# Performance work log

Measured on AMD Instinct MI355X. Metric: run time of the kernel, lower is better.

Reference implementation:

```python
import jax, jax.numpy as jnp
import numpy as np

B, S = 64, 1024
DC, DR, H, DA = 64, 64, 128, 128
NC, NQ, MC = 256, 10000, 4


def setup_inputs() -> dict:
    key = jax.random.key(0)
    ks = jax.random.split(key, 16)
    question_seq = jax.random.randint(ks[0], (B, S), 0, NQ)
    correctness_seq = jax.random.randint(ks[1], (B, S), 0, 2)
    q2c_table = jax.random.randint(ks[2], (NQ, MC), 0, NC)
    q2c_mask = jax.random.randint(ks[3], (NQ, MC), 0, 2).at[:, 0].set(1)  # >=1 concept per question
    sd = 0.02
    concept_embed = jax.random.normal(ks[4], (NC, DC), jnp.float32) * sd
    correctness_embed = jax.random.normal(ks[5], (2, DR), jnp.float32) * sd
    mlp_w = jax.random.normal(ks[6], (DA, H), jnp.float32) * (1.0 / np.sqrt(H))
    mlp_b = jnp.zeros((DA,), jnp.float32)
    sim_w = jax.random.normal(ks[7], (1, DA), jnp.float32) * (1.0 / np.sqrt(DA))
    DIN = DC + DR
    W_ih = jax.random.normal(ks[8], (3 * H, DIN), jnp.float32) * (1.0 / np.sqrt(H))
    b_ih = jnp.zeros((3 * H,), jnp.float32)
    W_hh = jax.random.normal(ks[9], (3 * H, H), jnp.float32) * (1.0 / np.sqrt(H))
    b_hh = jnp.zeros((3 * H,), jnp.float32)
    pred_w = jax.random.normal(ks[10], (1, 2 * H + DC), jnp.float32) * (1.0 / np.sqrt(2 * H + DC))
    pred_b = jnp.zeros((1,), jnp.float32)
    return dict(question_seq=question_seq, correctness_seq=correctness_seq,
                q2c_table=q2c_table, q2c_mask=q2c_mask,
                concept_embed=concept_embed, correctness_embed=correctness_embed,
                mlp_w=mlp_w, mlp_b=mlp_b, sim_w=sim_w,
                W_ih=W_ih, b_ih=b_ih, W_hh=W_hh, b_hh=b_hh,
                pred_w=pred_w, pred_b=pred_b)


def _concept_emb(question_seq, q2c_table, q2c_mask, concept_embed):
    # fused question->concept embedding: masked mean over mapped concepts
    cids = q2c_table[question_seq]                      # [B,S,MC]
    m = q2c_mask[question_seq].astype(jnp.float32)      # [B,S,MC]
    ce = concept_embed[cids]                            # [B,S,MC,DC]
    return (ce * m[..., None]).sum(2) / jnp.clip(m.sum(2), 1.0)[..., None]


def _gru(x, W_ih, b_ih, W_hh, b_hh):
    # torch nn.GRU equations, batch_first; x: [B,S,DIN] -> [B,S,H]
    Xp = jnp.einsum('bsd,gd->bsg', x, W_ih) + b_ih      # [B,S,3H]
    h0 = jnp.zeros((x.shape[0], H), x.dtype)

    def step(h, gi):
        gh = h @ W_hh.T + b_hh
        i_r, i_z, i_n = jnp.split(gi, 3, axis=-1)
        h_r, h_z, h_n = jnp.split(gh, 3, axis=-1)
        r = jax.nn.sigmoid(i_r + h_r)
        z = jax.nn.sigmoid(i_z + h_z)
        n = jnp.tanh(i_n + r * h_n)
        h_new = (1.0 - z) * n + z * h
        return h_new, h_new

    _, hs = jax.lax.scan(step, h0, Xp.transpose(1, 0, 2))
    return hs.transpose(1, 0, 2)


def _attention(rnn_out, mlp_w, mlp_b, sim_w):
    # additive per-key score, causal softmax, bmm, exclusive cumsum, concat
    s = jnp.einsum('bsa,oa->bso', jnp.tanh(jnp.einsum('bsh,ah->bsa', rnn_out, mlp_w) + mlp_b), sim_w)[..., 0]  # [B,S]
    seq = rnn_out.shape[1]
    causal = jnp.tril(jnp.ones((seq, seq), bool))       # keep j<=i
    scores = jnp.where(causal[None], s[:, None, :], -jnp.inf)  # [B,S,S]
    alphas = jax.nn.softmax(scores, axis=-1)
    attn = jnp.einsum('bij,bjh->bih', alphas, rnn_out)  # [B,S,H]
    excl = jnp.cumsum(attn, axis=1) - attn              # exclusive cumsum
    return jnp.concatenate([excl, rnn_out], axis=-1)    # [B,S,2H]


def reference(question_seq, correctness_seq, q2c_table, q2c_mask,
              concept_embed, correctness_embed, mlp_w, mlp_b, sim_w,
              W_ih, b_ih, W_hh, b_hh, pred_w, pred_b):
    concept = _concept_emb(question_seq, q2c_table, q2c_mask, concept_embed)  # [B,S,DC]
    corr = correctness_embed[correctness_seq]                                  # [B,S,DR]
    cc = jnp.concatenate([concept, corr], -1)
    rc = jnp.concatenate([corr, concept], -1)
    inter = jnp.where((correctness_seq == 1)[..., None], cc, rc)               # [B,S,DC+DR]
    rnn_out = _gru(inter, W_ih, b_ih, W_hh, b_hh)                              # [B,S,H]
    latent = _attention(rnn_out, mlp_w, mlp_b, sim_w)                          # [B,S,2H]
    pin = jnp.concatenate([latent[:, :-1], concept[:, 1:]], axis=-1)           # [B,S-1,2H+DC]
    logits = jnp.einsum('bsd,od->bso', pin, pred_w) + pred_b
    return jax.nn.sigmoid(logits)[..., 0]                                      # [B,S-1]
```

## Files before the change

### kernel.cpp

```cpp
#include <hip/hip_runtime.h>
#include <hip/hip_bf16.h>
#include <cstdint>

#define BB 64
#define SS 1024
#define DCn 64
#define Hn 128
#define G3 384
#define HPITCH 144

using f32x4 = __attribute__((ext_vector_type(4))) float;
using bf16x8 = __attribute__((ext_vector_type(8))) short;

__device__ __forceinline__ float sigmoid_f(float x) {
  return __builtin_amdgcn_rcpf(1.0f + __expf(-x));
}
__device__ __forceinline__ float tanh_f(float x) {
  float xc = fminf(fmaxf(x, -15.0f), 15.0f);
  float t = __expf(-2.0f * xc);
  return (1.0f - t) * __builtin_amdgcn_rcpf(1.0f + t);
}
__device__ __forceinline__ short f2bf(float x) {
  union { float f; uint32_t u; } v; v.f = x;
  uint32_t r = v.u + 0x7FFFu + ((v.u >> 16) & 1u);
  return (short)(r >> 16);
}
__device__ __forceinline__ float bf2f(ushort u) {
  union { uint32_t i; float f; } v; v.i = (uint32_t)u << 16; return v.f;
}
__device__ __forceinline__ float sel4(f32x4 v, int q) {
  float t0 = (q & 1) ? v[1] : v[0];
  float t1 = (q & 1) ? v[3] : v[2];
  return (q & 2) ? t1 : t0;
}

#define LDS_BARRIER() do {                                   \
    asm volatile("s_waitcnt lgkmcnt(0)" ::: "memory");       \
    __builtin_amdgcn_s_barrier();                            \
    __builtin_amdgcn_sched_barrier(0);                       \
  } while (0)

__global__ __launch_bounds__(256) void convw_kernel(
    const float* __restrict__ W_ih, const float* __restrict__ mlp_w,
    ushort* __restrict__ Wihb, ushort* __restrict__ mlpwb) {
  int i = blockIdx.x * 256 + threadIdx.x;
  if (i < 49152) Wihb[i] = (ushort)f2bf(W_ih[i]);
  else mlpwb[i - 49152] = (ushort)f2bf(mlp_w[i - 49152]);
}

__global__ __launch_bounds__(256) void embed_kernel(
    const int* __restrict__ qseq, const int* __restrict__ cseq,
    const int* __restrict__ q2c, const int* __restrict__ q2cm,
    const float* __restrict__ cemb, const float* __restrict__ remb,
    ushort* __restrict__ interb, float* __restrict__ concept) {
  int pos = blockIdx.x * 2 + (threadIdx.x >> 7);
  int d = threadIdx.x & 127;
  int q = qseq[pos];
  int corr = cseq[pos];
  float val;
  if (d < 64) {
    float acc = 0.f, msum = 0.f;
#pragma unroll
    for (int c = 0; c < 4; ++c) {
      int id = q2c[q * 4 + c];
      float m = (float)q2cm[q * 4 + c];
      acc += m * cemb[id * 64 + d];
      msum += m;
    }
    val = acc / fmaxf(msum, 1.0f);
    concept[(size_t)pos * 64 + d] = val;
  } else {
    val = remb[corr * 64 + (d - 64)];
  }
  int slot = (corr == 1) ? d : ((d < 64) ? d + 64 : d - 64);
  interb[(size_t)pos * 128 + slot] = (ushort)f2bf(val);
}

template <bool AF32, bool OUTBF>
__global__ __launch_bounds__(256) void gemm_mfma_kernel(
    const void* __restrict__ Ap, const ushort* __restrict__ Bp,
    const float* __restrict__ bias, void* __restrict__ Cp, int N) {
  __shared__ bf16x8 Al[64][16];
  __shared__ bf16x8 Bl[64][16];
  const int m0 = blockIdx.x * 64, n0 = blockIdx.y * 64;
  const int tid = threadIdx.x;
  const int row = tid >> 2, j0 = (tid & 3) * 4;
  if (AF32) {
    const float* A = (const float*)Ap + (size_t)(m0 + row) * 128 + j0 * 8;
#pragma unroll
    for (int jj = 0; jj < 4; ++jj) {
      f32x4 lo = *(const f32x4*)(A + jj * 8);
      f32x4 hi = *(const f32x4*)(A + jj * 8 + 4);
      bf16x8 v;
#pragma unroll
      for (int q = 0; q < 4; ++q) { v[q] = f2bf(lo[q]); v[4 + q] = f2bf(hi[q]); }
      Al[row][(j0 + jj) ^ (row & 15)] = v;
    }
  } else {
    const bf16x8* A = (const bf16x8*)Ap + (size_t)(m0 + row) * 16 + j0;
#pragma unroll
    for (int jj = 0; jj < 4; ++jj) Al[row][(j0 + jj) ^ (row & 15)] = A[jj];
  }
  {
    const bf16x8* Bg = (const bf16x8*)Bp + (size_t)(n0 + row) * 16 + j0;
#pragma unroll
    for (int jj = 0; jj < 4; ++jj) Bl[row][(j0 + jj) ^ (row & 15)] = Bg[jj];
  }
  __syncthreads();
  const int w = tid >> 6, lane = tid & 63, ln = lane & 15, cc = lane >> 4;
  bf16x8 bf[4];
#pragma unroll
  for (int ks = 0; ks < 4; ++ks) bf[ks] = Bl[w * 16 + ln][(ks * 4 + cc) ^ ln];
  f32x4 C0 = {0,0,0,0}, C1 = {0,0,0,0}, C2 = {0,0,0,0}, C3 = {0,0,0,0};
#pragma unroll
  for (int ks = 0; ks < 4; ++ks) {
    bf16x8 a0 = Al[0 * 16 + ln][(ks * 4 + cc) ^ ln];
    bf16x8 a1 = Al[1 * 16 + ln][(ks * 4 + cc) ^ ln];
    bf16x8 a2 = Al[2 * 16 + ln][(ks * 4 + cc) ^ ln];
    bf16x8 a3 = Al[3 * 16 + ln][(ks * 4 + cc) ^ ln];
    C0 = __builtin_amdgcn_mfma_f32_16x16x32_bf16(a0, bf[ks], C0, 0, 0, 0);
    C1 = __builtin_amdgcn_mfma_f32_16x16x32_bf16(a1, bf[ks], C1, 0, 0, 0);
    C2 = __builtin_amdgcn_mfma_f32_16x16x32_bf16(a2, bf[ks], C2, 0, 0, 0);
    C3 = __builtin_amdgcn_mfma_f32_16x16x32_bf16(a3, bf[ks], C3, 0, 0, 0);
  }
  const float bv = bias[n0 + w * 16 + ln];
  const size_t ncol = n0 + w * 16 + ln;
#pragma unroll
  for (int rt = 0; rt < 4; ++rt) {
    f32x4 Cf = (rt == 0) ? C0 : (rt == 1) ? C1 : (rt == 2) ? C2 : C3;
#pragma unroll
    for (int q = 0; q < 4; ++q) {
      float v = Cf[q] + bv;
      size_t idx = (size_t)(m0 + rt * 16 + cc * 4 + q) * N + ncol;
      if (OUTBF) ((ushort*)Cp)[idx] = (ushort)f2bf(v);
      else ((float*)Cp)[idx] = v;
    }
  }
}

__global__ __attribute__((amdgpu_flat_work_group_size(512, 512)))
__attribute__((amdgpu_waves_per_eu(2, 2))) void gru_kernel(
    const ushort* __restrict__ Xp, const float* __restrict__ W_hh,
    const float* __restrict__ b_hh, float* __restrict__ rnn_out) {
  const int tid = threadIdx.x;
  const int w = tid >> 6;
  const int lane = tid & 63;
  const int ln = lane & 15;
  const int c = lane >> 4;
  const int bl = ln & 3;
  const int qs = ln >> 2;
  const int b0 = blockIdx.x * 4;

  __shared__ alignas(16) short hlds[2][4 * HPITCH];

  bf16x8 wf[3][4];
#pragma unroll
  for (int gt = 0; gt < 3; ++gt) {
    const float* wr = W_hh + (size_t)(gt * 128 + w * 16 + ln) * 128 + c * 8;
#pragma unroll
    for (int ks = 0; ks < 4; ++ks) {
      bf16x8 f;
#pragma unroll
      for (int j = 0; j < 8; ++j) f[j] = f2bf(wr[ks * 32 + j]);
      wf[gt][ks] = f;
    }
  }
  const f32x4 br = *(const f32x4*)(b_hh + w * 16 + c * 4);
  const f32x4 bz = *(const f32x4*)(b_hh + 128 + w * 16 + c * 4);
  const f32x4 bn = *(const f32x4*)(b_hh + 256 + w * 16 + c * 4);

  for (int i = tid; i < 576; i += 512) ((uint32_t*)hlds)[i] = 0;

  const int dim = w * 16 + c * 4 + qs;
  const ushort* xs = Xp + (size_t)(b0 + bl) * SS * G3 + dim;
  float* rsp = rnn_out + (size_t)(b0 + bl) * SS * Hn + dim;

  ushort xr0 = xs[0], xz0 = xs[128], xn0 = xs[256];
  ushort xr1 = xs[G3 + 0], xz1 = xs[G3 + 128], xn1 = xs[G3 + 256];
  const ushort* xpf = xs + 2 * (size_t)G3;

  float h_old = 0.0f;
  LDS_BARRIER();

#define GRU_STEP(RB, XR, XZ, XN)                                             \
  {                                                                          \
    const short* hr = hlds[RB] + bl * HPITCH;                                \
    bf16x8 h0 = *(const bf16x8*)(hr + 0 * 32 + c * 8);                       \
    bf16x8 h1 = *(const bf16x8*)(hr + 1 * 32 + c * 8);                       \
    bf16x8 h2 = *(const bf16x8*)(hr + 2 * 32 + c * 8);                       \
    bf16x8 h3 = *(const bf16x8*)(hr + 3 * 32 + c * 8);                       \
    ushort pr = xpf[0], pz = xpf[128], pn = xpf[256];                        \
    xpf += G3;                                                               \
    __builtin_amdgcn_s_setprio(1);                                           \
    f32x4 ar = br, az = bz, an = bn;                                         \
    ar = __builtin_amdgcn_mfma_f32_16x16x32_bf16(wf[0][0], h0, ar, 0, 0, 0); \
    an = __builtin_amdgcn_mfma_f32_16x16x32_bf16(wf[2][0], h0, an, 0, 0, 0); \
    ar = __builtin_amdgcn_mfma_f32_16x16x32_bf16(wf[0][1], h1, ar, 0, 0, 0); \
    an = __builtin_amdgcn_mfma_f32_16x16x32_bf16(wf[2][1], h1, an, 0, 0, 0); \
    ar = __builtin_amdgcn_mfma_f32_16x16x32_bf16(wf[0][2], h2, ar, 0, 0, 0); \
    an = __builtin_amdgcn_mfma_f32_16x16x32_bf16(wf[2][2], h2, an, 0, 0, 0); \
    ar = __builtin_amdgcn_mfma_f32_16x16x32_bf16(wf[0][3], h3, ar, 0, 0, 0); \
    an = __builtin_amdgcn_mfma_f32_16x16x32_bf16(wf[2][3], h3, an, 0, 0, 0); \
    az = __builtin_amdgcn_mfma_f32_16x16x32_bf16(wf[1][0], h0, az, 0, 0, 0); \
    az = __builtin_amdgcn_mfma_f32_16x16x32_bf16(wf[1][1], h1, az, 0, 0, 0); \
    az = __builtin_amdgcn_mfma_f32_16x16x32_bf16(wf[1][2], h2, az, 0, 0, 0); \
    az = __builtin_amdgcn_mfma_f32_16x16x32_bf16(wf[1][3], h3, az, 0, 0, 0); \
    __builtin_amdgcn_s_setprio(0);                                           \
    float ga = sel4(ar, qs), gz = sel4(az, qs), gn = sel4(an, qs);           \
    float r = sigmoid_f(bf2f(XR) + ga);                                      \
    float a = bf2f(XN) + r * gn;                                             \
    float e = __expf(-2.0f * a);                                             \
    float n = 2.0f * __builtin_amdgcn_rcpf(1.0f + e) - 1.0f;                 \
    float z = sigmoid_f(bf2f(XZ) + gz);                                      \
    float hn = n + z * (h_old - n);                                          \
    h_old = hn;                                                              \
    hlds[RB ^ 1][bl * HPITCH + dim] = f2bf(hn);                              \
    LDS_BARRIER();                                                           \
    *rsp = hn;                                                               \
    rsp += Hn;                                                               \
    XR = pr; XZ = pz; XN = pn;                                               \
  }

  for (int t = 0; t < SS; t += 2) {
    GRU_STEP(0, xr0, xz0, xn0)
    GRU_STEP(1, xr1, xz1, xn1)
  }
#undef GRU_STEP
}

__global__ __launch_bounds__(256) void score_kernel(
    const float* __restrict__ tmpA, const float* __restrict__ sim_w,
    float* __restrict__ s) {
  int pos = blockIdx.x * 4 + (threadIdx.x >> 6);
  int lane = threadIdx.x & 63;
  const float* row = tmpA + (size_t)pos * 128;
  float v = tanh_f(row[lane]) * sim_w[lane] +
            tanh_f(row[lane + 64]) * sim_w[lane + 64];
#pragma unroll
  for (int o = 32; o; o >>= 1) v += __shfl_down(v, o);
  if (lane == 0) s[pos] = v;
}

__global__ __launch_bounds__(64) void attn_kernel(
    const float* __restrict__ s, const float* __restrict__ rnn,
    float* __restrict__ excl) {
  const int b = blockIdx.x >> 1;
  const int h = ((blockIdx.x & 1) << 6) + threadIdx.x;
  const int tl = threadIdx.x;
  __shared__ float elds[SS];
  const float* sb = s + (size_t)b * SS;
  float m = -1e30f;
  for (int i = tl; i < SS; i += 64) m = fmaxf(m, sb[i]);
#pragma unroll
  for (int o = 32; o; o >>= 1) m = fmaxf(m, __shfl_xor(m, o));
  for (int i = tl; i < SS; i += 64) elds[i] = __expf(sb[i] - m);
  __syncthreads();

  const float* rb = rnn + (size_t)b * SS * Hn + h;
  float* eb = excl + (size_t)b * SS * Hn + h;
  float num = 0.f, den = 0.f, run = 0.f;
  float rcur = rb[0];
  for (int t = 0; t < SS; ++t) {
    float rnxt = (t < SS - 1) ? rb[(size_t)(t + 1) * Hn] : 0.0f;
    float e = elds[t];
    den += e;
    num += e * rcur;
    eb[(size_t)t * Hn] = run;
    run += num * __builtin_amdgcn_rcpf(den);
    rcur = rnxt;
  }
}

__global__ __launch_bounds__(256) void out_kernel(
    const float* __restrict__ excl, const float* __restrict__ rnn,
    const float* __restrict__ concept, const float* __restrict__ pred_w,
    const float* __restrict__ pred_b, float* __restrict__ out) {
  int idx = blockIdx.x * 4 + (threadIdx.x >> 6);
  int lane = threadIdx.x & 63;
  if (idx >= BB * (SS - 1)) return;
  int b = idx / (SS - 1), t = idx % (SS - 1);
  const float* e = excl + ((size_t)b * SS + t) * Hn;
  const float* r = rnn + ((size_t)b * SS + t) * Hn;
  const float* c = concept + ((size_t)b * SS + t + 1) * DCn;
  float v = e[lane] * pred_w[lane] + e[lane + 64] * pred_w[lane + 64] +
            r[lane] * pred_w[128 + lane] + r[lane + 64] * pred_w[192 + lane] +
            c[lane] * pred_w[256 + lane];
#pragma unroll
  for (int o = 32; o; o >>= 1) v += __shfl_down(v, o);
  if (lane == 0) out[idx] = sigmoid_f(v + pred_b[0]);
}

extern "C" void kernel_launch(void* const* d_in, const int* in_sizes, int n_in,
                              void* d_out, int out_size, void* d_ws, size_t ws_size,
                              hipStream_t stream) {
  const int* qseq = (const int*)d_in[0];
  const int* cseq = (const int*)d_in[1];
  const int* q2c = (const int*)d_in[2];
  const int* q2cm = (const int*)d_in[3];
  const float* cemb = (const float*)d_in[4];
  const float* remb = (const float*)d_in[5];
  const float* mlp_w = (const float*)d_in[6];
  const float* mlp_b = (const float*)d_in[7];
  const float* sim_w = (const float*)d_in[8];
  const float* W_ih = (const float*)d_in[9];
  const float* b_ih = (const float*)d_in[10];
  const float* W_hh = (const float*)d_in[11];
  const float* b_hh = (const float*)d_in[12];
  const float* pred_w = (const float*)d_in[13];
  const float* pred_b = (const float*)d_in[14];
  float* out = (float*)d_out;

  float* ws = (float*)d_ws;
  float* concept = ws;
  ushort* interb = (ushort*)(ws + 4194304);
  ushort* Xp = (ushort*)(ws + 8388608);
  float* rnn = ws + 20971520;
  ushort* Wihb = (ushort*)(ws + 29360128);
  ushort* mlpwb = (ushort*)(ws + 29384704);
  float* tmpA = ws + 29392896;
  float* sbuf = ws + 4194304;
  float* excl = ws + 8388608;

  convw_kernel<<<256, 256, 0, stream>>>(W_ih, mlp_w, Wihb, mlpwb);
  embed_kernel<<<32768, 256, 0, stream>>>(qseq, cseq, q2c, q2cm, cemb, remb,
                                          interb, concept);
  gemm_mfma_kernel<false, true><<<dim3(1024, 6), 256, 0, stream>>>(
      interb, Wihb, b_ih, Xp, 384);
  gru_kernel<<<16, 512, 0, stream>>>(Xp, W_hh, b_hh, rnn);
  gemm_mfma_kernel<true, false><<<dim3(1024, 2), 256, 0, stream>>>(
      rnn, mlpwb, mlp_b, tmpA, 128);
  score_kernel<<<16384, 256, 0, stream>>>(tmpA, sim_w, sbuf);
  attn_kernel<<<128, 64, 0, stream>>>(sbuf, rnn, excl);
  out_kernel<<<16368, 256, 0, stream>>>(excl, rnn, concept, pred_w, pred_b, out);
}
```

Baseline: 572.8 us.

## Project attention and prediction onto pred_w early and fuse score into MLP GEMM

The prediction dot-product is linear, so the code projects rnn_out onto the two pred_w halves as two extra output columns of the MLP GEMM (D1, D2). It also reduces concept to a scalar C3 inside the embed kernel. The attention prefix-sum then runs on scalars per batch, with a parallel scan for the softmax denominators, instead of over 128 hidden dims, and it produces the sigmoid output directly. The tanh and sim_w score reduction is fused into the GEMM epilogue, which removes the tmpA, excl and concept buffers and the score and out kernels. The trade-off is a serial scalar loop per batch on a single thread and bf16 rounding of the pred_w projection.

```diff
diff --git a/kernel.cpp b/kernel.cpp
--- a/kernel.cpp
+++ b/kernel.cpp
@@ -42,17 +42,24 @@
 
 __global__ __launch_bounds__(256) void convw_kernel(
     const float* __restrict__ W_ih, const float* __restrict__ mlp_w,
-    ushort* __restrict__ Wihb, ushort* __restrict__ mlpwb) {
+    const float* __restrict__ pred_w,
+    ushort* __restrict__ Wihb, ushort* __restrict__ Baug) {
   int i = blockIdx.x * 256 + threadIdx.x;
-  if (i < 49152) Wihb[i] = (ushort)f2bf(W_ih[i]);
-  else mlpwb[i - 49152] = (ushort)f2bf(mlp_w[i - 49152]);
+  if (i < 49152) { Wihb[i] = (ushort)f2bf(W_ih[i]); return; }
+  int j = i - 49152;
+  int r = j >> 7, k = j & 127;
+  float v = (r < 128) ? mlp_w[j]
+          : (r == 128) ? pred_w[k]
+          : (r == 129) ? pred_w[128 + k] : 0.0f;
+  Baug[j] = (ushort)f2bf(v);
 }
 
 __global__ __launch_bounds__(256) void embed_kernel(
     const int* __restrict__ qseq, const int* __restrict__ cseq,
     const int* __restrict__ q2c, const int* __restrict__ q2cm,
     const float* __restrict__ cemb, const float* __restrict__ remb,
-    ushort* __restrict__ interb, float* __restrict__ concept) {
+    const float* __restrict__ pred_w,
+    ushort* __restrict__ interb, float* __restrict__ C3) {
   int pos = blockIdx.x * 2 + (threadIdx.x >> 7);
   int d = threadIdx.x & 127;
   int q = qseq[pos];
@@ -68,7 +75,10 @@
       msum += m;
     }
     val = acc / fmaxf(msum, 1.0f);
-    concept[(size_t)pos * 64 + d] = val;
+    float p3 = val * pred_w[256 + d];
+#pragma unroll
+    for (int o = 32; o; o >>= 1) p3 += __shfl_down(p3, o);
+    if (d == 0) C3[pos] = p3;
   } else {
     val = remb[corr * 64 + (d - 64)];
   }
@@ -76,65 +86,47 @@
   interb[(size_t)pos * 128 + slot] = (ushort)f2bf(val);
 }
 
-template <bool AF32, bool OUTBF>
 __global__ __launch_bounds__(256) void gemm_mfma_kernel(
-    const void* __restrict__ Ap, const ushort* __restrict__ Bp,
-    const float* __restrict__ bias, void* __restrict__ Cp, int N) {
+    const ushort* __restrict__ Ap, const ushort* __restrict__ Bp,
+    const float* __restrict__ bias, ushort* __restrict__ Cp, int N) {
   __shared__ bf16x8 Al[64][16];
   __shared__ bf16x8 Bl[64][16];
   const int m0 = blockIdx.x * 64, n0 = blockIdx.y * 64;
   const int tid = threadIdx.x;
   const int row = tid >> 2, j0 = (tid & 3) * 4;
-  if (AF32) {
-    const float* A = (const float*)Ap + (size_t)(m0 + row) * 128 + j0 * 8;
-#pragma unroll
-    for (int jj = 0; jj < 4; ++jj) {
-      f32x4 lo = *(const f32x4*)(A + jj * 8);
-      f32x4 hi = *(const f32x4*)(A + jj * 8 + 4);
-      bf16x8 v;
-#pragma unroll
-      for (int q = 0; q < 4; ++q) { v[q] = f2bf(lo[q]); v[4 + q] = f2bf(hi[q]); }
-      Al[row][(j0 + jj) ^ (row & 15)] = v;
-    }
-  } else {
+  {
     const bf16x8* A = (const bf16x8*)Ap + (size_t)(m0 + row) * 16 + j0;
 #pragma unroll
     for (int jj = 0; jj < 4; ++jj) Al[row][(j0 + jj) ^ (row & 15)] = A[jj];
-  }
-  {
     const bf16x8* Bg = (const bf16x8*)Bp + (size_t)(n0 + row) * 16 + j0;
 #pragma unroll
     for (int jj = 0; jj < 4; ++jj) Bl[row][(j0 + jj) ^ (row & 15)] = Bg[jj];
   }
   __syncthreads();
   const int w = tid >> 6, lane = tid & 63, ln = lane & 15, cc = lane >> 4;
-  bf16x8 bf[4];
-#pragma unroll
-  for (int ks = 0; ks < 4; ++ks) bf[ks] = Bl[w * 16 + ln][(ks * 4 + cc) ^ ln];
-  f32x4 C0 = {0,0,0,0}, C1 = {0,0,0,0}, C2 = {0,0,0,0}, C3 = {0,0,0,0};
+  bf16x8 bfr[4];
+#pragma unroll
+  for (int ks = 0; ks < 4; ++ks) bfr[ks] = Bl[w * 16 + ln][(ks * 4 + cc) ^ ln];
+  f32x4 C0 = {0,0,0,0}, C1 = {0,0,0,0}, C2 = {0,0,0,0}, C3v = {0,0,0,0};
 #pragma unroll
   for (int ks = 0; ks < 4; ++ks) {
     bf16x8 a0 = Al[0 * 16 + ln][(ks * 4 + cc) ^ ln];
     bf16x8 a1 = Al[1 * 16 + ln][(ks * 4 + cc) ^ ln];
     bf16x8 a2 = Al[2 * 16 + ln][(ks * 4 + cc) ^ ln];
     bf16x8 a3 = Al[3 * 16 + ln][(ks * 4 + cc) ^ ln];
-    C0 = __builtin_amdgcn_mfma_f32_16x16x32_bf16(a0, bf[ks], C0, 0, 0, 0);
-    C1 = __builtin_amdgcn_mfma_f32_16x16x32_bf16(a1, bf[ks], C1, 0, 0, 0);
-    C2 = __builtin_amdgcn_mfma_f32_16x16x32_bf16(a2, bf[ks], C2, 0, 0, 0);
-    C3 = __builtin_amdgcn_mfma_f32_16x16x32_bf16(a3, bf[ks], C3, 0, 0, 0);
+    C0 = __builtin_amdgcn_mfma_f32_16x16x32_bf16(a0, bfr[ks], C0, 0, 0, 0);
+    C1 = __builtin_amdgcn_mfma_f32_16x16x32_bf16(a1, bfr[ks], C1, 0, 0, 0);
+    C2 = __builtin_amdgcn_mfma_f32_16x16x32_bf16(a2, bfr[ks], C2, 0, 0, 0);
+    C3v = __builtin_amdgcn_mfma_f32_16x16x32_bf16(a3, bfr[ks], C3v, 0, 0, 0);
   }
   const float bv = bias[n0 + w * 16 + ln];
   const size_t ncol = n0 + w * 16 + ln;
 #pragma unroll
   for (int rt = 0; rt < 4; ++rt) {
-    f32x4 Cf = (rt == 0) ? C0 : (rt == 1) ? C1 : (rt == 2) ? C2 : C3;
-#pragma unroll
-    for (int q = 0; q < 4; ++q) {
-      float v = Cf[q] + bv;
-      size_t idx = (size_t)(m0 + rt * 16 + cc * 4 + q) * N + ncol;
-      if (OUTBF) ((ushort*)Cp)[idx] = (ushort)f2bf(v);
-      else ((float*)Cp)[idx] = v;
-    }
+    f32x4 Cf = (rt == 0) ? C0 : (rt == 1) ? C1 : (rt == 2) ? C2 : C3v;
+#pragma unroll
+    for (int q = 0; q < 4; ++q)
+      Cp[(size_t)(m0 + rt * 16 + cc * 4 + q) * N + ncol] = (ushort)f2bf(Cf[q] + bv);
   }
 }
 
@@ -228,66 +220,160 @@
 #undef GRU_STEP
 }
 
-__global__ __launch_bounds__(256) void score_kernel(
-    const float* __restrict__ tmpA, const float* __restrict__ sim_w,
-    float* __restrict__ s) {
-  int pos = blockIdx.x * 4 + (threadIdx.x >> 6);
-  int lane = threadIdx.x & 63;
-  const float* row = tmpA + (size_t)pos * 128;
-  float v = tanh_f(row[lane]) * sim_w[lane] +
-            tanh_f(row[lane + 64]) * sim_w[lane + 64];
-#pragma unroll
-  for (int o = 32; o; o >>= 1) v += __shfl_down(v, o);
-  if (lane == 0) s[pos] = v;
-}
-
-__global__ __launch_bounds__(64) void attn_kernel(
-    const float* __restrict__ s, const float* __restrict__ rnn,
-    float* __restrict__ excl) {
-  const int b = blockIdx.x >> 1;
-  const int h = ((blockIdx.x & 1) << 6) + threadIdx.x;
-  const int tl = threadIdx.x;
+__global__ __launch_bounds__(256) void gemm_score_kernel(
+    const float* __restrict__ rnn, const ushort* __restrict__ Baug,
+    const float* __restrict__ mlp_b, const float* __restrict__ sim_w,
+    float* __restrict__ s, float* __restrict__ D1, float* __restrict__ D2) {
+  __shared__ bf16x8 Al[64][16];
+  __shared__ bf16x8 Bl[144][16];
+  __shared__ float srow[64][4];
+  const int m0 = blockIdx.x * 64;
+  const int tid = threadIdx.x;
+  {
+    const int row = tid >> 2, j0 = (tid & 3) * 4;
+    const float* A = rnn + (size_t)(m0 + row) * 128 + j0 * 8;
+#pragma unroll
+    for (int jj = 0; jj < 4; ++jj) {
+      f32x4 lo = *(const f32x4*)(A + jj * 8);
+      f32x4 hi = *(const f32x4*)(A + jj * 8 + 4);
+      bf16x8 v;
+#pragma unroll
+      for (int q = 0; q < 4; ++q) { v[q] = f2bf(lo[q]); v[4 + q] = f2bf(hi[q]); }
+      Al[row][(j0 + jj) ^ (row & 15)] = v;
+    }
+  }
+  {
+    const bf16x8* Bg = (const bf16x8*)Baug;
+    for (int i = tid; i < 144 * 16; i += 256) {
+      int r = i >> 4, j = i & 15;
+      Bl[r][j ^ (r & 15)] = Bg[i];
+    }
+  }
+  __syncthreads();
+  const int w = tid >> 6, lane = tid & 63, ln = lane & 15, cc = lane >> 4;
+  float racc[4][4] = {};
+  for (int nt = w; nt < 9; nt += 4) {
+    bf16x8 bfr[4];
+#pragma unroll
+    for (int ks = 0; ks < 4; ++ks) bfr[ks] = Bl[nt * 16 + ln][(ks * 4 + cc) ^ ln];
+    f32x4 C0 = {0,0,0,0}, C1 = {0,0,0,0}, C2 = {0,0,0,0}, C3v = {0,0,0,0};
+#pragma unroll
+    for (int ks = 0; ks < 4; ++ks) {
+      bf16x8 a0 = Al[0 * 16 + ln][(ks * 4 + cc) ^ ln];
+      bf16x8 a1 = Al[1 * 16 + ln][(ks * 4 + cc) ^ ln];
+      bf16x8 a2 = Al[2 * 16 + ln][(ks * 4 + cc) ^ ln];
+      bf16x8 a3 = Al[3 * 16 + ln][(ks * 4 + cc) ^ ln];
+      C0 = __builtin_amdgcn_mfma_f32_16x16x32_bf16(a0, bfr[ks], C0, 0, 0, 0);
+      C1 = __builtin_amdgcn_mfma_f32_16x16x32_bf16(a1, bfr[ks], C1, 0, 0, 0);
+      C2 = __builtin_amdgcn_mfma_f32_16x16x32_bf16(a2, bfr[ks], C2, 0, 0, 0);
+      C3v = __builtin_amdgcn_mfma_f32_16x16x32_bf16(a3, bfr[ks], C3v, 0, 0, 0);
+    }
+    if (nt < 8) {
+      const int col = nt * 16 + ln;
+      const float bv = mlp_b[col];
+      const float sw = sim_w[col];
+#pragma unroll
+      for (int rt = 0; rt < 4; ++rt) {
+        f32x4 Cf = (rt == 0) ? C0 : (rt == 1) ? C1 : (rt == 2) ? C2 : C3v;
+#pragma unroll
+        for (int q = 0; q < 4; ++q)
+          racc[rt][q] += tanh_f(Cf[q] + bv) * sw;
+      }
+    } else if (ln < 2) {
+      float* Dp = (ln == 0) ? D1 : D2;
+#pragma unroll
+      for (int rt = 0; rt < 4; ++rt) {
+        f32x4 Cf = (rt == 0) ? C0 : (rt == 1) ? C1 : (rt == 2) ? C2 : C3v;
+#pragma unroll
+        for (int q = 0; q < 4; ++q)
+          Dp[m0 + rt * 16 + cc * 4 + q] = Cf[q];
+      }
+    }
+  }
+#pragma unroll
+  for (int o = 1; o <= 8; o <<= 1)
+#pragma unroll
+    for (int rt = 0; rt < 4; ++rt)
+#pragma unroll
+      for (int q = 0; q < 4; ++q)
+        racc[rt][q] += __shfl_xor(racc[rt][q], o);
+  if (ln == 0)
+#pragma unroll
+    for (int rt = 0; rt < 4; ++rt)
+#pragma unroll
+      for (int q = 0; q < 4; ++q)
+        srow[rt * 16 + cc * 4 + q][w] = racc[rt][q];
+  __syncthreads();
+  if (tid < 64)
+    s[m0 + tid] = srow[tid][0] + srow[tid][1] + srow[tid][2] + srow[tid][3];
+}
+
+__global__ __launch_bounds__(128) void attn_final_kernel(
+    const float* __restrict__ s, const float* __restrict__ D1,
+    const float* __restrict__ D2, const float* __restrict__ C3,
+    const float* __restrict__ pred_b, float* __restrict__ out) {
+  const int b = blockIdx.x;
+  const int tid = threadIdx.x;
   __shared__ float elds[SS];
+  __shared__ float rcpd[SS];
+  __shared__ float d1l[SS];
+  __shared__ float dcl[SS];
+  __shared__ float red[2];
+  __shared__ float wtot[2];
+  const float pb = pred_b[0];
   const float* sb = s + (size_t)b * SS;
+  const float* d1b = D1 + (size_t)b * SS;
+  const float* d2b = D2 + (size_t)b * SS;
+  const float* c3b = C3 + (size_t)b * SS;
   float m = -1e30f;
-  for (int i = tl; i < SS; i += 64) m = fmaxf(m, sb[i]);
+  for (int i = tid; i < SS; i += 128) m = fmaxf(m, sb[i]);
 #pragma unroll
   for (int o = 32; o; o >>= 1) m = fmaxf(m, __shfl_xor(m, o));
-  for (int i = tl; i < SS; i += 64) elds[i] = __expf(sb[i] - m);
-  __syncthreads();
-
-  const float* rb = rnn + (size_t)b * SS * Hn + h;
-  float* eb = excl + (size_t)b * SS * Hn + h;
-  float num = 0.f, den = 0.f, run = 0.f;
-  float rcur = rb[0];
-  for (int t = 0; t < SS; ++t) {
-    float rnxt = (t < SS - 1) ? rb[(size_t)(t + 1) * Hn] : 0.0f;
-    float e = elds[t];
-    den += e;
-    num += e * rcur;
-    eb[(size_t)t * Hn] = run;
-    run += num * __builtin_amdgcn_rcpf(den);
-    rcur = rnxt;
-  }
-}
-
-__global__ __launch_bounds__(256) void out_kernel(
-    const float* __restrict__ excl, const float* __restrict__ rnn,
-    const float* __restrict__ concept, const float* __restrict__ pred_w,
-    const float* __restrict__ pred_b, float* __restrict__ out) {
-  int idx = blockIdx.x * 4 + (threadIdx.x >> 6);
-  int lane = threadIdx.x & 63;
-  if (idx >= BB * (SS - 1)) return;
-  int b = idx / (SS - 1), t = idx % (SS - 1);
-  const float* e = excl + ((size_t)b * SS + t) * Hn;
-  const float* r = rnn + ((size_t)b * SS + t) * Hn;
-  const float* c = concept + ((size_t)b * SS + t + 1) * DCn;
-  float v = e[lane] * pred_w[lane] + e[lane + 64] * pred_w[lane + 64] +
-            r[lane] * pred_w[128 + lane] + r[lane + 64] * pred_w[192 + lane] +
-            c[lane] * pred_w[256 + lane];
-#pragma unroll
-  for (int o = 32; o; o >>= 1) v += __shfl_down(v, o);
-  if (lane == 0) out[idx] = sigmoid_f(v + pred_b[0]);
+  if ((tid & 63) == 0) red[tid >> 6] = m;
+  __syncthreads();
+  m = fmaxf(red[0], red[1]);
+  for (int i = tid; i < SS; i += 128) {
+    elds[i] = __expf(sb[i] - m);
+    d1l[i] = d1b[i];
+    dcl[i] = d2b[i] + ((i < SS - 1) ? c3b[i + 1] : 0.0f) + pb;
+  }
+  __syncthreads();
+  {
+    const int base = tid * 8;
+    float v[8];
+    float run = 0.f;
+#pragma unroll
+    for (int k = 0; k < 8; ++k) { run += elds[base + k]; v[k] = run; }
+    float tot = run, sc = tot;
+#pragma unroll
+    for (int o = 1; o < 64; o <<= 1) {
+      float u = __shfl_up(sc, o);
+      if ((tid & 63) >= o) sc += u;
+    }
+    if ((tid & 63) == 63) wtot[tid >> 6] = sc;
+    __syncthreads();
+    float excl = sc - tot;
+    if (tid >= 64) excl += wtot[0];
+#pragma unroll
+    for (int k = 0; k < 8; ++k)
+      rcpd[base + k] = __builtin_amdgcn_rcpf(v[k] + excl);
+  }
+  __syncthreads();
+  float P_num = 0.f, P_run = 0.f;
+  float* ob = out + (size_t)b * (SS - 1);
+  for (int t = 0; t < SS; t += 4) {
+    f32x4 e4 = *(const f32x4*)&elds[t];
+    f32x4 r4 = *(const f32x4*)&rcpd[t];
+    f32x4 d4 = *(const f32x4*)&d1l[t];
+    f32x4 c4 = *(const f32x4*)&dcl[t];
+#pragma unroll
+    for (int k = 0; k < 4; ++k) {
+      P_num += e4[k] * d4[k];
+      float v = sigmoid_f(P_run + c4[k]);
+      if (tid == 0 && (t + k) < SS - 1) ob[t + k] = v;
+      P_run += P_num * r4[k];
+    }
+  }
 }
 
 extern "C" void kernel_launch(void* const* d_in, const int* in_sizes, int n_in,
@@ -311,25 +397,22 @@
   float* out = (float*)d_out;
 
   float* ws = (float*)d_ws;
-  float* concept = ws;
-  ushort* interb = (ushort*)(ws + 4194304);
-  ushort* Xp = (ushort*)(ws + 8388608);
-  float* rnn = ws + 20971520;
-  ushort* Wihb = (ushort*)(ws + 29360128);
-  ushort* mlpwb = (ushort*)(ws + 29384704);
-  float* tmpA = ws + 29392896;
-  float* sbuf = ws + 4194304;
-  float* excl = ws + 8388608;
-
-  convw_kernel<<<256, 256, 0, stream>>>(W_ih, mlp_w, Wihb, mlpwb);
+  ushort* interb = (ushort*)ws;
+  ushort* Xp = (ushort*)(ws + 4194304);
+  float* rnn = ws + 16777216;
+  ushort* Wihb = (ushort*)(ws + 25165824);
+  ushort* Baug = (ushort*)(ws + 25190400);
+  float* sbuf = ws + 25199616;
+  float* D1 = ws + 25265152;
+  float* D2 = ws + 25330688;
+  float* C3 = ws + 25396224;
+
+  convw_kernel<<<264, 256, 0, stream>>>(W_ih, mlp_w, pred_w, Wihb, Baug);
   embed_kernel<<<32768, 256, 0, stream>>>(qseq, cseq, q2c, q2cm, cemb, remb,
-                                          interb, concept);
-  gemm_mfma_kernel<false, true><<<dim3(1024, 6), 256, 0, stream>>>(
-      interb, Wihb, b_ih, Xp, 384);
+                                          pred_w, interb, C3);
+  gemm_mfma_kernel<<<dim3(1024, 6), 256, 0, stream>>>(interb, Wihb, b_ih, Xp, 384);
   gru_kernel<<<16, 512, 0, stream>>>(Xp, W_hh, b_hh, rnn);
-  gemm_mfma_kernel<true, false><<<dim3(1024, 2), 256, 0, stream>>>(
-      rnn, mlpwb, mlp_b, tmpA, 128);
-  score_kernel<<<16384, 256, 0, stream>>>(tmpA, sim_w, sbuf);
-  attn_kernel<<<128, 64, 0, stream>>>(sbuf, rnn, excl);
-  out_kernel<<<16368, 256, 0, stream>>>(excl, rnn, concept, pred_w, pred_b, out);
-}
+  gemm_score_kernel<<<1024, 256, 0, stream>>>(rnn, Baug, mlp_b, sim_w,
+                                              sbuf, D1, D2);
+  attn_final_kernel<<<64, 128, 0, stream>>>(sbuf, D1, D2, C3, pred_b, out);
+}
```

After: 509.4 us. 11.1% less time.
